# Optimization experiments

Measured on AMD Instinct MI355X. Metric: run time of the kernel, lower is better.

Reference implementation:

```python
import jax, jax.numpy as jnp
import numpy as np

def _round_ste(x):
    # StraightThrough: forward = round, backward = identity
    return x + jax.lax.stop_gradient(jnp.round(x) - x)

def setup_inputs() -> dict:
    key = jax.random.key(0)
    k1, k2, k3, k4, k5 = jax.random.split(key, 5)
    in_f, out_f, n_tok = 4096, 4096, 8192
    return {
        "input": jax.random.normal(k1, (n_tok, in_f), dtype=jnp.float32),
        "weight": jax.random.normal(k2, (out_f, in_f), dtype=jnp.float32),
        "bias": jax.random.normal(k3, (out_f,), dtype=jnp.float32),
        "w_scale": jax.random.uniform(k4, (1,), dtype=jnp.float32),
        "b_scale": jax.random.uniform(k5, (1,), dtype=jnp.float32),
    }

def reference(input, weight, bias, w_scale, b_scale):
    # straight-through rounding of quantized latents (use_straight_through=True, compress_bias=True)
    w_q = _round_ste(weight)
    b_q = _round_ste(bias)
    # decoder: per-tensor affine dequantization
    w_dec = w_scale * w_q          # [out, in]
    b_dec = b_scale * b_q          # [out]
    # F.linear: input @ weight.T + bias
    return jnp.einsum('ni,oi->no', input, w_dec) + b_dec
```

## Files before the change

kernel.cpp:

```cpp
#include <hip/hip_runtime.h>
#include <stdint.h>


using bf16x8   = __attribute__((ext_vector_type(8))) __bf16;
using floatx16 = __attribute__((ext_vector_type(16))) float;
using us8      = __attribute__((ext_vector_type(8))) unsigned short;
using us4      = __attribute__((ext_vector_type(4))) unsigned short;

__device__ __forceinline__ unsigned short f2bf_rne(float x) {
    unsigned int u = __float_as_uint(x);
    return (unsigned short)((u + 0x7fffu + ((u >> 16) & 1u)) >> 16);
}

__device__ __forceinline__ void stage16(const unsigned short* g, unsigned short* l) {
    __builtin_amdgcn_global_load_lds(
        (__attribute__((address_space(1))) void*)g,
        (__attribute__((address_space(3))) void*)l,
        16, 0, 0);
}

__global__ __launch_bounds__(256) void cvt_both(
    const float* __restrict__ inA, unsigned short* __restrict__ outA, long long nA4,
    const float* __restrict__ inB, unsigned short* __restrict__ outB, long long nB4) {
    const long long i = (long long)blockIdx.x * 256 + threadIdx.x;
    if (i < nA4) {
        float4 v = ((const float4*)inA)[i];
        us4 o = { f2bf_rne(v.x), f2bf_rne(v.y), f2bf_rne(v.z), f2bf_rne(v.w) };
        ((us4*)outA)[i] = o;
    } else {
        const long long j = i - nA4;
        if (j < nB4) {
            float4 v = ((const float4*)inB)[j];
            us4 o = { f2bf_rne(rintf(v.x)), f2bf_rne(rintf(v.y)),
                      f2bf_rne(rintf(v.z)), f2bf_rne(rintf(v.w)) };
            ((us4*)outB)[j] = o;
        }
    }
}

__global__ __launch_bounds__(512) void gemm256_fm(
    const unsigned short* __restrict__ A,
    const unsigned short* __restrict__ B,
    const float* __restrict__ bias,
    const float* __restrict__ wscale_p,
    const float* __restrict__ bscale_p,
    float* __restrict__ C,
    int M, int N, int K) {
    constexpr int BK   = 64;
    constexpr int TILE = 16384;
    __shared__ unsigned short ldsA[2 * TILE];
    __shared__ unsigned short ldsB[2 * TILE];

    const int tid  = threadIdx.x;
    const int wave = tid >> 6;
    const int lane = tid & 63;

    const int nbx = N >> 8;
    int wg;
    {
        const int cpx = (int)gridDim.x >> 3;
        wg = ((int)blockIdx.x & 7) * cpx + ((int)blockIdx.x >> 3);
    }
    const int bm = (wg / nbx) << 8;
    const int bn = (wg % nbx) << 8;

    const int wr    = wave >> 2;
    const int wc    = wave & 3;
    const int col   = lane & 31;
    const int khalf = lane >> 5;

    const int q   = wave >> 1;
    const int mb1 = (q & 1) + ((q >> 1) << 2);
    const int mb3 = mb1 + 2;
    const int kb  = (wave & 1) << 1;

    const unsigned short* gAl = A + (size_t)(bm + col) * K + (khalf << 3);
    const unsigned short* gBl = B + (size_t)(bn + col) * K + (khalf << 3);

    const int lane16 = lane << 3;

    const float wsc = wscale_p[0];
    const float bsc = bscale_p[0];
    float badd[2];
#pragma unroll
    for (int ni = 0; ni < 2; ++ni)
        badd[ni] = bsc * rintf(bias[bn + wc * 64 + ni * 32 + col]);

    const int NT = K >> 6;

#define ABLK(buf, mb, ks) ((buf) * TILE + (((mb) * 4 + (ks)) << 9))
#define BBLK(buf, nb, ks) ((buf) * TILE + (((nb) * 4 + (ks)) << 9))
#define ST_A(buf, mb, ks, kt) \
    stage16(gAl + (size_t)((mb) * 32) * K + (kt) + (ks) * 16, &ldsA[ABLK(buf, mb, ks)])
#define ST_B(buf, nb, ks, kt) \
    stage16(gBl + (size_t)((nb) * 32) * K + (kt) + (ks) * 16, &ldsB[BBLK(buf, nb, ks)])
#define RD_A(buf, mb, ks) \
    __builtin_bit_cast(bf16x8, *(const us8*)&ldsA[ABLK(buf, mb, ks) + lane16])
#define RD_B(buf, nb, ks) \
    __builtin_bit_cast(bf16x8, *(const us8*)&ldsB[BBLK(buf, nb, ks) + lane16])

#pragma unroll
    for (int i = 0; i < 4; ++i) ST_B(0, wave, i, 0);
    ST_A(0, mb1, kb, 0);
    ST_A(0, mb1, kb + 1, 0);
    ST_A(0, mb3, kb, 0);
    ST_A(0, mb3, kb + 1, 0);
    asm volatile("s_waitcnt vmcnt(2)" ::: "memory");
    __builtin_amdgcn_s_barrier();
    __builtin_amdgcn_sched_barrier(0);

    floatx16 acc[4][2] = {};

#define PH_BAR_LGKM()                                        \
    __builtin_amdgcn_s_barrier();                            \
    asm volatile("s_waitcnt lgkmcnt(0)" ::: "memory");       \
    __builtin_amdgcn_sched_barrier(0);

#define PH_MFMA(MIB, KSB)                                                     \
    __builtin_amdgcn_s_setprio(1);                                            \
    _Pragma("unroll") for (int k2 = 0; k2 < 2; ++k2)                          \
        _Pragma("unroll") for (int m2 = 0; m2 < 2; ++m2)                      \
            _Pragma("unroll") for (int ni = 0; ni < 2; ++ni)                  \
                acc[(MIB) + m2][ni] = __builtin_amdgcn_mfma_f32_32x32x16_bf16(\
                    Af[m2][k2], Bf[ni][(KSB) + k2], acc[(MIB) + m2][ni],      \
                    0, 0, 0);                                                 \
    __builtin_amdgcn_s_setprio(0);                                            \
    __builtin_amdgcn_sched_barrier(0);

    for (int t = 0; t < NT; ++t) {
        const int rb_ = t & 1;
        const int sb_ = (t + 1) & 1;
        const int kt1 = (t + 1) * BK;
        const bool st = (t + 1 < NT);

        bf16x8 Af[2][2];
        bf16x8 Bf[2][4];

#pragma unroll
        for (int m2 = 0; m2 < 2; ++m2)
#pragma unroll
            for (int k2 = 0; k2 < 2; ++k2) Af[m2][k2] = RD_A(rb_, wr * 4 + m2, k2);
#pragma unroll
        for (int ni = 0; ni < 2; ++ni)
#pragma unroll
            for (int k2 = 0; k2 < 2; ++k2) Bf[ni][k2] = RD_B(rb_, wc * 2 + ni, k2);
        if (st) {
#pragma unroll
            for (int i = 0; i < 4; ++i) ST_B(sb_, wave, i, kt1);
        }
        PH_BAR_LGKM()
        PH_MFMA(0, 0)
        __builtin_amdgcn_s_barrier();
        __builtin_amdgcn_sched_barrier(0);

#pragma unroll
        for (int m2 = 0; m2 < 2; ++m2)
#pragma unroll
            for (int k2 = 0; k2 < 2; ++k2) Af[m2][k2] = RD_A(rb_, wr * 4 + m2, 2 + k2);
#pragma unroll
        for (int ni = 0; ni < 2; ++ni)
#pragma unroll
            for (int k2 = 0; k2 < 2; ++k2) Bf[ni][2 + k2] = RD_B(rb_, wc * 2 + ni, 2 + k2);
        if (st) {
            ST_A(sb_, mb1, kb, kt1);
            ST_A(sb_, mb1, kb + 1, kt1);
        }
        PH_BAR_LGKM()
        PH_MFMA(0, 2)
        if (st) { asm volatile("s_waitcnt vmcnt(6)" ::: "memory"); }
        else    { asm volatile("s_waitcnt vmcnt(0)" ::: "memory"); }
        __builtin_amdgcn_s_barrier();
        __builtin_amdgcn_sched_barrier(0);

#pragma unroll
        for (int m2 = 0; m2 < 2; ++m2)
#pragma unroll
            for (int k2 = 0; k2 < 2; ++k2) Af[m2][k2] = RD_A(rb_, wr * 4 + 2 + m2, k2);
        PH_BAR_LGKM()
        PH_MFMA(2, 0)
        __builtin_amdgcn_s_barrier();
        __builtin_amdgcn_sched_barrier(0);

#pragma unroll
        for (int m2 = 0; m2 < 2; ++m2)
#pragma unroll
            for (int k2 = 0; k2 < 2; ++k2) Af[m2][k2] = RD_A(rb_, wr * 4 + 2 + m2, 2 + k2);
        if (st) {
            ST_A(sb_, mb3, kb, kt1);
            ST_A(sb_, mb3, kb + 1, kt1);
        }
        PH_BAR_LGKM()
        PH_MFMA(2, 2)
        if (st) { asm volatile("s_waitcnt vmcnt(2)" ::: "memory"); }
        __builtin_amdgcn_s_barrier();
        __builtin_amdgcn_sched_barrier(0);
    }

#undef PH_BAR_LGKM
#undef PH_MFMA
#undef ABLK
#undef BBLK
#undef ST_A
#undef ST_B
#undef RD_A
#undef RD_B

    const int rb = khalf << 2;
#pragma unroll
    for (int mi = 0; mi < 4; ++mi) {
#pragma unroll
        for (int ni = 0; ni < 2; ++ni) {
            const int n = bn + wc * 64 + ni * 32 + col;
#pragma unroll
            for (int reg = 0; reg < 16; ++reg) {
                const int m = bm + wr * 128 + mi * 32 + (reg & 3) + 8 * (reg >> 2) + rb;
                C[(size_t)m * N + n] = acc[mi][ni][reg] * wsc + badd[ni];
            }
        }
    }
}

__global__ __launch_bounds__(256) void gemm_bf16_bt(
    const unsigned short* __restrict__ A,
    const unsigned short* __restrict__ B,
    const float* __restrict__ bias,
    const float* __restrict__ wscale_p,
    const float* __restrict__ bscale_p,
    float* __restrict__ C,
    int M, int N, int K) {
    constexpr int BM = 128, BK = 64;
    __shared__ unsigned short ldsA[BM * BK];
    __shared__ unsigned short ldsB[BM * BK];

    const int tid  = threadIdx.x;
    const int wave = tid >> 6;
    const int lane = tid & 63;

    const int bm = blockIdx.y * BM;
    const int bn = blockIdx.x * BM;
    const int wm = (wave >> 1) * 64;
    const int wn = (wave & 1) * 64;

    const float wsc = wscale_p[0];
    const float bsc = bscale_p[0];

    const int col = lane & 31;
    const int khalf = lane >> 5;

    float badd[2];
#pragma unroll
    for (int ni = 0; ni < 2; ++ni)
        badd[ni] = bsc * rintf(bias[bn + wn + ni * 32 + col]);

    const int g_st = ((lane & 7) ^ (lane >> 3)) * 8;
    const unsigned short* gAp[4];
    const unsigned short* gBp[4];
    unsigned short* lA[4];
    unsigned short* lB[4];
#pragma unroll
    for (int i = 0; i < 4; ++i) {
        const int r = wave * 32 + i * 8 + (lane >> 3);
        gAp[i] = A + (size_t)(bm + r) * K + g_st;
        gBp[i] = B + (size_t)(bn + r) * K + g_st;
        lA[i] = &ldsA[(wave * 256 + i * 64) * 8];
        lB[i] = &ldsB[(wave * 256 + i * 64) * 8];
    }

    floatx16 acc[2][2] = {};

    for (int kt = 0; kt < K; kt += BK) {
#pragma unroll
        for (int i = 0; i < 4; ++i) {
            stage16(gAp[i] + kt, lA[i]);
            stage16(gBp[i] + kt, lB[i]);
        }
        __syncthreads();

#pragma unroll
        for (int ks = 0; ks < 4; ++ks) {
            const int gc = ks * 2 + khalf;
            const int slot = (gc ^ (lane & 7)) * 8;
            bf16x8 af[2], bfr[2];
#pragma unroll
            for (int mi = 0; mi < 2; ++mi) {
                const int off = (wm + mi * 32 + col) * BK + slot;
                af[mi] = __builtin_bit_cast(bf16x8, *(const us8*)&ldsA[off]);
            }
#pragma unroll
            for (int ni = 0; ni < 2; ++ni) {
                const int off = (wn + ni * 32 + col) * BK + slot;
                bfr[ni] = __builtin_bit_cast(bf16x8, *(const us8*)&ldsB[off]);
            }
#pragma unroll
            for (int mi = 0; mi < 2; ++mi)
#pragma unroll
                for (int ni = 0; ni < 2; ++ni)
                    acc[mi][ni] = __builtin_amdgcn_mfma_f32_32x32x16_bf16(
                        af[mi], bfr[ni], acc[mi][ni], 0, 0, 0);
        }
        __syncthreads();
    }

    const int rbase = 4 * khalf;
#pragma unroll
    for (int mi = 0; mi < 2; ++mi) {
#pragma unroll
        for (int ni = 0; ni < 2; ++ni) {
            const int n = bn + wn + ni * 32 + col;
#pragma unroll
            for (int reg = 0; reg < 16; ++reg) {
                const int m = bm + wm + mi * 32 + (reg & 3) + 8 * (reg >> 2) + rbase;
                C[(size_t)m * N + n] = acc[mi][ni][reg] * wsc + badd[ni];
            }
        }
    }
}

__global__ __launch_bounds__(256) void fallback_gemm(
    const float* __restrict__ A, const float* __restrict__ W,
    const float* __restrict__ bias, const float* __restrict__ wsp,
    const float* __restrict__ bsp, float* __restrict__ C, int M, int N, int K) {
    const int n = blockIdx.x * 256 + threadIdx.x;
    const int m = blockIdx.y;
    if (n >= N || m >= M) return;
    float s = 0.f;
    for (int k = 0; k < K; ++k)
        s += A[(size_t)m * K + k] * rintf(W[(size_t)n * K + k]);
    C[(size_t)m * N + n] = s * wsp[0] + bsp[0] * rintf(bias[n]);
}

extern "C" void kernel_launch(void* const* d_in, const int* in_sizes, int n_in,
                              void* d_out, int out_size, void* d_ws, size_t ws_size,
                              hipStream_t stream) {
    const float* input  = (const float*)d_in[0];
    const float* weight = (const float*)d_in[1];
    const float* bias   = (const float*)d_in[2];
    const float* wscale = (const float*)d_in[3];
    const float* bscale = (const float*)d_in[4];
    float* out = (float*)d_out;

    const int N = in_sizes[2];
    const int K = in_sizes[1] / N;
    const int M = in_sizes[0] / K;

    const size_t needA = (size_t)M * K * sizeof(unsigned short);
    const size_t needB = (size_t)N * K * sizeof(unsigned short);

    if (ws_size >= needA + needB && (M % 128) == 0 && (N % 128) == 0 &&
        (K % 64) == 0) {
        unsigned short* Abf = (unsigned short*)d_ws;
        unsigned short* Bbf = (unsigned short*)((char*)d_ws + needA);
        const long long nA4 = (long long)M * K / 4;
        const long long nB4 = (long long)N * K / 4;
        const long long nthr = nA4 + nB4;
        cvt_both<<<(unsigned)((nthr + 255) / 256), 256, 0, stream>>>(
            input, Abf, nA4, weight, Bbf, nB4);

        const int nwg256 = (M / 256) * (N / 256);
        if ((M % 256) == 0 && (N % 256) == 0 && (K / 64) >= 1 &&
            (nwg256 % 8) == 0) {
            gemm256_fm<<<dim3(nwg256), 512, 0, stream>>>(
                Abf, Bbf, bias, wscale, bscale, out, M, N, K);
        } else {
            dim3 grid(N / 128, M / 128);
            gemm_bf16_bt<<<grid, 256, 0, stream>>>(Abf, Bbf, bias, wscale,
                                                   bscale, out, M, N, K);
        }
    } else {
        dim3 grid((N + 255) / 256, M);
        fallback_gemm<<<grid, 256, 0, stream>>>(input, weight, bias, wscale, bscale, out, M, N, K);
    }
}
```

Measured before the change: 630.7 us.

## Pre-swizzle bf16 operands into MFMA fragment layout for contiguous tile staging

```diff
diff --git a/kernel.cpp b/kernel.cpp
--- a/kernel.cpp
+++ b/kernel.cpp
@@ -17,6 +17,42 @@
         (__attribute__((address_space(1))) void*)g,
         (__attribute__((address_space(3))) void*)l,
         16, 0, 0);
+}
+
+template<bool DO_RINT>
+__global__ __launch_bounds__(256) void cvt_frag(
+    const float* __restrict__ in, unsigned short* __restrict__ out, int K) {
+    const int KS16 = K >> 4;
+    const int rg   = blockIdx.x;
+    const int w    = threadIdx.x >> 6;
+    const int lane = threadIdx.x & 63;
+    const int r5   = lane & 31;
+    const int kh   = lane >> 5;
+    const int QF   = KS16 >> 2;
+    const int bks  = blockIdx.y * QF;
+
+    const float* src = in + (size_t)(rg * 32 + r5) * K + kh * 8;
+    unsigned short* dst = out + ((size_t)(rg * KS16) << 9) + (lane << 3);
+
+    for (int i = w; i < QF; i += 4) {
+        const int ksg = bks + i;
+        const float* s = src + ksg * 16;
+        float4 v0 = *(const float4*)(s);
+        float4 v1 = *(const float4*)(s + 4);
+        us8 o;
+        if (DO_RINT) {
+            o = us8{ f2bf_rne(rintf(v0.x)), f2bf_rne(rintf(v0.y)),
+                     f2bf_rne(rintf(v0.z)), f2bf_rne(rintf(v0.w)),
+                     f2bf_rne(rintf(v1.x)), f2bf_rne(rintf(v1.y)),
+                     f2bf_rne(rintf(v1.z)), f2bf_rne(rintf(v1.w)) };
+        } else {
+            o = us8{ f2bf_rne(v0.x), f2bf_rne(v0.y),
+                     f2bf_rne(v0.z), f2bf_rne(v0.w),
+                     f2bf_rne(v1.x), f2bf_rne(v1.y),
+                     f2bf_rne(v1.z), f2bf_rne(v1.w) };
+        }
+        *(us8*)(dst + ((size_t)ksg << 9)) = o;
+    }
 }
 
 __global__ __launch_bounds__(256) void cvt_both(
@@ -38,7 +74,7 @@
     }
 }
 
-__global__ __launch_bounds__(512) void gemm256_fm(
+__global__ __launch_bounds__(512) void gemm256_fg(
     const unsigned short* __restrict__ A,
     const unsigned short* __restrict__ B,
     const float* __restrict__ bias,
@@ -46,7 +82,6 @@
     const float* __restrict__ bscale_p,
     float* __restrict__ C,
     int M, int N, int K) {
-    constexpr int BK   = 64;
     constexpr int TILE = 16384;
     __shared__ unsigned short ldsA[2 * TILE];
     __shared__ unsigned short ldsB[2 * TILE];
@@ -69,13 +104,12 @@
     const int col   = lane & 31;
     const int khalf = lane >> 5;
 
-    const int q   = wave >> 1;
-    const int mb1 = (q & 1) + ((q >> 1) << 2);
-    const int mb3 = mb1 + 2;
-    const int kb  = (wave & 1) << 1;
-
-    const unsigned short* gAl = A + (size_t)(bm + col) * K + (khalf << 3);
-    const unsigned short* gBl = B + (size_t)(bn + col) * K + (khalf << 3);
+    const int KS16 = K >> 4;
+    const int bmb  = bm >> 5;
+    const int bnb  = bn >> 5;
+
+    const unsigned short* gAf = A + (lane << 3);
+    const unsigned short* gBf = B + (lane << 3);
 
     const int lane16 = lane << 3;
 
@@ -90,21 +124,21 @@
 
 #define ABLK(buf, mb, ks) ((buf) * TILE + (((mb) * 4 + (ks)) << 9))
 #define BBLK(buf, nb, ks) ((buf) * TILE + (((nb) * 4 + (ks)) << 9))
-#define ST_A(buf, mb, ks, kt) \
-    stage16(gAl + (size_t)((mb) * 32) * K + (kt) + (ks) * 16, &ldsA[ABLK(buf, mb, ks)])
-#define ST_B(buf, nb, ks, kt) \
-    stage16(gBl + (size_t)((nb) * 32) * K + (kt) + (ks) * 16, &ldsB[BBLK(buf, nb, ks)])
+#define ST_A(buf, mb, ks, kf) \
+    stage16(gAf + (((size_t)(bmb + (mb)) * KS16 + (kf)) << 9), &ldsA[ABLK(buf, mb, ks)])
+#define ST_B(buf, nb, ks, kf) \
+    stage16(gBf + (((size_t)(bnb + (nb)) * KS16 + (kf)) << 9), &ldsB[BBLK(buf, nb, ks)])
 #define RD_A(buf, mb, ks) \
     __builtin_bit_cast(bf16x8, *(const us8*)&ldsA[ABLK(buf, mb, ks) + lane16])
 #define RD_B(buf, nb, ks) \
     __builtin_bit_cast(bf16x8, *(const us8*)&ldsB[BBLK(buf, nb, ks) + lane16])
 
 #pragma unroll
-    for (int i = 0; i < 4; ++i) ST_B(0, wave, i, 0);
-    ST_A(0, mb1, kb, 0);
-    ST_A(0, mb1, kb + 1, 0);
-    ST_A(0, mb3, kb, 0);
-    ST_A(0, mb3, kb + 1, 0);
+    for (int i = 0; i < 4; ++i) ST_B(0, wave, i, i);
+    ST_A(0, wave, 0, 0);
+    ST_A(0, wave, 1, 1);
+    ST_A(0, wave, 2, 2);
+    ST_A(0, wave, 3, 3);
     asm volatile("s_waitcnt vmcnt(2)" ::: "memory");
     __builtin_amdgcn_s_barrier();
     __builtin_amdgcn_sched_barrier(0);
@@ -130,7 +164,7 @@
     for (int t = 0; t < NT; ++t) {
         const int rb_ = t & 1;
         const int sb_ = (t + 1) & 1;
-        const int kt1 = (t + 1) * BK;
+        const int kf1 = (t + 1) << 2;
         const bool st = (t + 1 < NT);
 
         bf16x8 Af[2][2];
@@ -146,10 +180,12 @@
             for (int k2 = 0; k2 < 2; ++k2) Bf[ni][k2] = RD_B(rb_, wc * 2 + ni, k2);
         if (st) {
 #pragma unroll
-            for (int i = 0; i < 4; ++i) ST_B(sb_, wave, i, kt1);
+            for (int i = 0; i < 4; ++i) ST_B(sb_, wave, i, kf1 + i);
         }
         PH_BAR_LGKM()
         PH_MFMA(0, 0)
+        if (st) { asm volatile("s_waitcnt vmcnt(4)" ::: "memory"); }
+        else    { asm volatile("s_waitcnt vmcnt(0)" ::: "memory"); }
         __builtin_amdgcn_s_barrier();
         __builtin_amdgcn_sched_barrier(0);
 
@@ -162,13 +198,11 @@
 #pragma unroll
             for (int k2 = 0; k2 < 2; ++k2) Bf[ni][2 + k2] = RD_B(rb_, wc * 2 + ni, 2 + k2);
         if (st) {
-            ST_A(sb_, mb1, kb, kt1);
-            ST_A(sb_, mb1, kb + 1, kt1);
+            ST_A(sb_, wave, 0, kf1);
+            ST_A(sb_, wave, 1, kf1 + 1);
         }
         PH_BAR_LGKM()
         PH_MFMA(0, 2)
-        if (st) { asm volatile("s_waitcnt vmcnt(6)" ::: "memory"); }
-        else    { asm volatile("s_waitcnt vmcnt(0)" ::: "memory"); }
         __builtin_amdgcn_s_barrier();
         __builtin_amdgcn_sched_barrier(0);
 
@@ -186,8 +220,8 @@
 #pragma unroll
             for (int k2 = 0; k2 < 2; ++k2) Af[m2][k2] = RD_A(rb_, wr * 4 + 2 + m2, 2 + k2);
         if (st) {
-            ST_A(sb_, mb3, kb, kt1);
-            ST_A(sb_, mb3, kb + 1, kt1);
+            ST_A(sb_, wave, 2, kf1 + 2);
+            ST_A(sb_, wave, 3, kf1 + 3);
         }
         PH_BAR_LGKM()
         PH_MFMA(2, 2)
@@ -345,9 +379,19 @@
 
     const size_t needA = (size_t)M * K * sizeof(unsigned short);
     const size_t needB = (size_t)N * K * sizeof(unsigned short);
-
-    if (ws_size >= needA + needB && (M % 128) == 0 && (N % 128) == 0 &&
-        (K % 64) == 0) {
+    const bool big = ws_size >= needA + needB;
+
+    const int nwg256 = (M / 256) * (N / 256);
+
+    if (big && (M % 256) == 0 && (N % 256) == 0 && (K % 256) == 0 &&
+        (nwg256 % 8) == 0) {
+        unsigned short* Abf = (unsigned short*)d_ws;
+        unsigned short* Bbf = (unsigned short*)((char*)d_ws + needA);
+        cvt_frag<false><<<dim3(M / 32, 4), 256, 0, stream>>>(input, Abf, K);
+        cvt_frag<true><<<dim3(N / 32, 4), 256, 0, stream>>>(weight, Bbf, K);
+        gemm256_fg<<<dim3(nwg256), 512, 0, stream>>>(
+            Abf, Bbf, bias, wscale, bscale, out, M, N, K);
+    } else if (big && (M % 128) == 0 && (N % 128) == 0 && (K % 64) == 0) {
         unsigned short* Abf = (unsigned short*)d_ws;
         unsigned short* Bbf = (unsigned short*)((char*)d_ws + needA);
         const long long nA4 = (long long)M * K / 4;
@@ -355,17 +399,9 @@
         const long long nthr = nA4 + nB4;
         cvt_both<<<(unsigned)((nthr + 255) / 256), 256, 0, stream>>>(
             input, Abf, nA4, weight, Bbf, nB4);
-
-        const int nwg256 = (M / 256) * (N / 256);
-        if ((M % 256) == 0 && (N % 256) == 0 && (K / 64) >= 1 &&
-            (nwg256 % 8) == 0) {
-            gemm256_fm<<<dim3(nwg256), 512, 0, stream>>>(
-                Abf, Bbf, bias, wscale, bscale, out, M, N, K);
-        } else {
-            dim3 grid(N / 128, M / 128);
-            gemm_bf16_bt<<<grid, 256, 0, stream>>>(Abf, Bbf, bias, wscale,
-                                                   bscale, out, M, N, K);
-        }
+        dim3 grid(N / 128, M / 128);
+        gemm_bf16_bt<<<grid, 256, 0, stream>>>(Abf, Bbf, bias, wscale,
+                                               bscale, out, M, N, K);
     } else {
         dim3 grid((N + 255) / 256, M);
         fallback_gemm<<<grid, 256, 0, stream>>>(input, weight, bias, wscale, bscale, out, M, N, K);
```

After: 541.6 us. 14.1% less time.
